# Kernel tuning notes

Hardware: AMD Instinct MI355X
Metric: run time of the kernel (lower is better)

## Reference

```python
import jax, jax.numpy as jnp
import numpy as np


def setup_inputs() -> dict:
    key = jax.random.key(0)
    kq, kk, kv = jax.random.split(key, 3)
    B, L, Q, H, E = 8, 128, 8, 8, 64
    S, P = 128, 8
    queries = jax.random.normal(kq, (B, L, Q, H, E), dtype=jnp.float32)
    keys = jax.random.normal(kk, (B, S, P, H, E), dtype=jnp.float32)
    values = jax.random.normal(kv, (B, S, P, H, E), dtype=jnp.float32)
    attn_mask = jnp.zeros((1,), dtype=bool)  # unused by the module
    return {"queries": queries, "keys": keys, "values": values, "attn_mask": attn_mask}


def reference(queries, keys, values, attn_mask):
    # queries: [B,L,Q,H,E]; keys/values: [B,S,P,H,E]
    B, L, Q, H, E = queries.shape
    S, P = values.shape[1], values.shape[2]
    scale = 1.0 / np.sqrt(E).astype(np.float32)
    # scores: [B,S,P,L,Q,H]
    scores = jnp.einsum('blqhe,bsphe->bsplqh', queries, keys)
    # softmax over joint (S,P) axis
    scaled = (scale * scores).reshape(B, S * P, L, Q, H)
    attn = jax.nn.softmax(scaled, axis=1).reshape(B, S, P, L, Q, H)
    # dropout is identity in eval / with p=0.0
    V = jnp.einsum('bsphe,bsplqh->blqhe', values, attn)
    return V
```

## Files before the change

kernel.cpp:

```cpp
#include <hip/hip_runtime.h>
#include <hip/hip_bf16.h>

typedef __attribute__((ext_vector_type(4))) float f32x4;
typedef __attribute__((ext_vector_type(16))) float f32x16;
typedef __attribute__((ext_vector_type(8))) short bf16x8;
typedef __attribute__((ext_vector_type(4))) unsigned u32x4;

#define MFMA32(a, b, c) __builtin_amdgcn_mfma_f32_32x32x16_bf16(a, b, c, 0, 0, 0)
#define EXP2(x) __builtin_amdgcn_exp2f(x)

constexpr int NQ = 1024;
constexpr int NK = 1024;
constexpr int RS = 512;
constexpr int Ec = 64;
constexpr int KT = 128;
constexpr int NT = NK / KT;
constexpr float QSCALE2 = 0.125f * 1.4426950408889634f;

__device__ __forceinline__ short f2bf(float x) {
    return (short)__builtin_bit_cast(unsigned short, __float2bfloat16(x));
}

__device__ __forceinline__ bf16x8 pack2(float4 a, float4 b) {
    bf16x8 r;
    r[0] = f2bf(a.x); r[1] = f2bf(a.y); r[2] = f2bf(a.z); r[3] = f2bf(a.w);
    r[4] = f2bf(b.x); r[5] = f2bf(b.y); r[6] = f2bf(b.z); r[7] = f2bf(b.w);
    return r;
}

__device__ __forceinline__ bf16x8 pack2s(float4 a, float4 b, float s) {
    bf16x8 r;
    r[0] = f2bf(a.x * s); r[1] = f2bf(a.y * s); r[2] = f2bf(a.z * s); r[3] = f2bf(a.w * s);
    r[4] = f2bf(b.x * s); r[5] = f2bf(b.y * s); r[6] = f2bf(b.z * s); r[7] = f2bf(b.w * s);
    return r;
}

__device__ __forceinline__ unsigned cvtpk(float a, float b) {
    unsigned lo = (unsigned short)__builtin_bit_cast(unsigned short, __float2bfloat16(a));
    unsigned hi = (unsigned short)__builtin_bit_cast(unsigned short, __float2bfloat16(b));
    return lo | (hi << 16);
}

__device__ __forceinline__ void gload16(const short* src, short* dst) {
    __builtin_amdgcn_global_load_lds((const __attribute__((address_space(1))) void*)src,
                                     (__attribute__((address_space(3))) void*)dst, 16, 0, 0);
}

__global__ __launch_bounds__(256, 4)
void cvt_kv(const float* __restrict__ Kg, const float* __restrict__ Vg,
            short* __restrict__ Kbf, short* __restrict__ Vt) {
    __shared__ __attribute__((aligned(16))) short Vl[64][72];
    const int tid  = threadIdx.x;
    const int head = blockIdx.x >> 4;
    const int kb   = blockIdx.x & 15;
    const int b    = head >> 3, h = head & 7;
    const int row  = tid >> 2, q = tid & 3;

    const size_t gin = (((size_t)(b * NK + kb * 64 + row)) * 8 + h) * 64 + q * 16;
    const float4* kp = (const float4*)(Kg + gin);
    float4 k0 = kp[0], k1 = kp[1], k2 = kp[2], k3 = kp[3];
    short* kout = Kbf + ((size_t)head * NK + kb * 64 + row) * 64 + q * 16;
    ((bf16x8*)kout)[0] = pack2(k0, k1);
    ((bf16x8*)kout)[1] = pack2(k2, k3);

    const float4* vp = (const float4*)(Vg + gin);
    float4 v0 = vp[0], v1 = vp[1], v2 = vp[2], v3 = vp[3];
    const float vv[16] = {v0.x, v0.y, v0.z, v0.w, v1.x, v1.y, v1.z, v1.w,
                          v2.x, v2.y, v2.z, v2.w, v3.x, v3.y, v3.z, v3.w};
#pragma unroll
    for (int j = 0; j < 16; ++j) Vl[q * 16 + j][row] = f2bf(vv[j]);
    __syncthreads();
    short* vout = Vt + ((size_t)head * Ec + row) * NK + kb * 64 + q * 16;
    ((bf16x8*)vout)[0] = *(const bf16x8*)&Vl[row][q * 16];
    ((bf16x8*)vout)[1] = *(const bf16x8*)&Vl[row][q * 16 + 8];
}

__global__ __launch_bounds__(512, 4)
void fully_attn_kernel(const float* __restrict__ Qg, const short* __restrict__ Kbf,
                       const short* __restrict__ Vt, float* __restrict__ Og) {
    __shared__ __attribute__((aligned(16))) short Kl[2][KT][64];
    __shared__ __attribute__((aligned(16))) short Vl[2][64][KT];

    const int tid  = threadIdx.x;
    const int lane = tid & 63;
    const int wv   = tid >> 6;
    const int grp  = wv & 3;
    const int par  = wv >> 2;
    const int ql   = lane & 31;
    const int hi   = lane >> 5;
    const int swz  = (lane & 7) << 4;

    const int bid  = blockIdx.x;
    const int head = (bid & 7) * 8 + (bid >> 6);
    const int qb   = (bid >> 3) & 7;
    const int b    = head >> 3, h = head & 7;

    const size_t headQ = (size_t)b * NQ * RS + (size_t)h * Ec;
    const short* Kh = Kbf + (size_t)head * NK * Ec;
    const short* Vh = Vt + (size_t)head * Ec * NK;

    const int qrow = qb * 128 + grp * 32 + ql;
    const float* qp = Qg + headQ + (size_t)qrow * RS;
    bf16x8 qf[4];
#pragma unroll
    for (int j = 0; j < 4; ++j) {
        const float4* q4 = (const float4*)(qp + j * 16 + hi * 8);
        qf[j] = pack2s(q4[0], q4[1], QSCALE2);
    }

    const int krow8 = lane >> 3;
    const int kj    = (lane & 7) ^ krow8;
    const int vrow4 = lane >> 4;

#define STAGE_K(buf, tt)                                                          \
    {                                                                             \
        _Pragma("unroll")                                                         \
        for (int s = 0; s < 2; ++s)                                               \
            gload16(Kh + (size_t)((tt) * KT + wv * 16 + s * 8 + krow8) * 64 +     \
                        kj * 8,                                                   \
                    &Kl[buf][wv * 16 + s * 8][0]);                                \
    }

#define STAGE_V(buf, tt)                                                          \
    {                                                                             \
        _Pragma("unroll")                                                         \
        for (int s = 0; s < 2; ++s)                                               \
            gload16(Vh + (size_t)(wv * 8 + s * 4 + vrow4) * NK + (tt) * KT +      \
                        (((lane & 15) ^ ((s * 4 + vrow4) & 7)) * 8),              \
                    &Vl[buf][wv * 8 + s * 4][0]);                                 \
    }

    STAGE_K(0, 0);
    STAGE_V(0, 0);
    __syncthreads();

    float l_r = 0.0f;
    f32x16 o0 = (f32x16)(0.0f), o1 = (f32x16)(0.0f);

    int cur = 0;
    for (int t = 0; t < NT; ++t) {
        if (t + 1 < NT) { STAGE_K(cur ^ 1, t + 1); STAGE_V(cur ^ 1, t + 1); }

        f32x16 p[2];
#pragma unroll
        for (int kt = 0; kt < 2; ++kt) {
            const char* kr = (const char*)&Kl[cur][par * 64 + kt * 32 + ql][0];
            bf16x8 kf0 = *(const bf16x8*)(kr + ((0 * 32 + hi * 16) ^ swz));
            bf16x8 kf1 = *(const bf16x8*)(kr + ((1 * 32 + hi * 16) ^ swz));
            bf16x8 kf2 = *(const bf16x8*)(kr + ((2 * 32 + hi * 16) ^ swz));
            bf16x8 kf3 = *(const bf16x8*)(kr + ((3 * 32 + hi * 16) ^ swz));
            __builtin_amdgcn_s_setprio(1);
            f32x16 acc = MFMA32(kf0, qf[0], (f32x16)(0.0f));
            acc = MFMA32(kf1, qf[1], acc);
            acc = MFMA32(kf2, qf[2], acc);
            acc = MFMA32(kf3, qf[3], acc);
            __builtin_amdgcn_s_setprio(0);
            p[kt] = acc;
        }

        float rs0 = 0.f, rs1 = 0.f, rs2 = 0.f, rs3 = 0.f;
#pragma unroll
        for (int kt = 0; kt < 2; ++kt)
#pragma unroll
            for (int i = 0; i < 16; i += 4) {
                float e0 = EXP2(p[kt][i + 0]);
                float e1 = EXP2(p[kt][i + 1]);
                float e2 = EXP2(p[kt][i + 2]);
                float e3 = EXP2(p[kt][i + 3]);
                p[kt][i + 0] = e0; p[kt][i + 1] = e1;
                p[kt][i + 2] = e2; p[kt][i + 3] = e3;
                rs0 += e0; rs1 += e1; rs2 += e2; rs3 += e3;
            }
        l_r += (rs0 + rs1) + (rs2 + rs3);

        const char* vr0 = (const char*)&Vl[cur][ql][0];
        const char* vr1 = (const char*)&Vl[cur][32 + ql][0];
        __builtin_amdgcn_s_setprio(1);
#pragma unroll
        for (int m = 0; m < 4; ++m) {
            const int kt = m >> 1, r0 = (m & 1) * 8;
            unsigned a0 = cvtpk(p[kt][r0 + 0], p[kt][r0 + 1]);
            unsigned a1 = cvtpk(p[kt][r0 + 2], p[kt][r0 + 3]);
            unsigned b0 = cvtpk(p[kt][r0 + 4], p[kt][r0 + 5]);
            unsigned b1 = cvtpk(p[kt][r0 + 6], p[kt][r0 + 7]);
            asm("v_permlane32_swap_b32 %0, %1" : "+v"(a0), "+v"(b0));
            asm("v_permlane32_swap_b32 %0, %1" : "+v"(a1), "+v"(b1));
            u32x4 w = {a0, a1, b0, b1};
            bf16x8 pf = __builtin_bit_cast(bf16x8, w);
            const int cb = (par * 128 + m * 32 + hi * 16) ^ swz;
            bf16x8 v0 = *(const bf16x8*)(vr0 + cb);
            bf16x8 v1 = *(const bf16x8*)(vr1 + cb);
            o0 = MFMA32(v0, pf, o0);
            o1 = MFMA32(v1, pf, o1);
        }
        __builtin_amdgcn_s_setprio(0);

        __syncthreads();
        cur ^= 1;
    }

    l_r += __shfl_xor(l_r, 32);

    float* scrO = (float*)&Kl[0][0][0];
    float* scrL = (float*)&Vl[0][0][0];
    const int slot = grp * 64 + lane;
    if (par == 1) {
#pragma unroll
        for (int i = 0; i < 16; ++i) {
            scrO[i * 256 + slot]        = o0[i];
            scrO[(16 + i) * 256 + slot] = o1[i];
        }
        scrL[slot] = l_r;
    }
    __syncthreads();
    if (par == 0) {
        const float inv = 1.0f / (l_r + scrL[slot]);
        float* op = Og + headQ + (size_t)qrow * RS;
#pragma unroll
        for (int bnk = 0; bnk < 4; ++bnk) {
            float4 s0, s1;
#pragma unroll
            for (int j = 0; j < 4; ++j) {
                const int i = bnk * 4 + j;
                ((float*)&s0)[j] = (o0[i] + scrO[i * 256 + slot]) * inv;
                ((float*)&s1)[j] = (o1[i] + scrO[(16 + i) * 256 + slot]) * inv;
            }
            *(float4*)(op + bnk * 8 + hi * 4)      = s0;
            *(float4*)(op + 32 + bnk * 8 + hi * 4) = s1;
        }
    }
}

extern "C" void kernel_launch(void* const* d_in, const int* in_sizes, int n_in,
                              void* d_out, int out_size, void* d_ws, size_t ws_size,
                              hipStream_t stream) {
    const float* Qg = (const float*)d_in[0];
    const float* Kg = (const float*)d_in[1];
    const float* Vg = (const float*)d_in[2];
    float* Og = (float*)d_out;

    short* Kbf = (short*)d_ws;
    short* Vt  = (short*)d_ws + (size_t)64 * NK * Ec;

    hipLaunchKernelGGL(cvt_kv, dim3(64 * 16), dim3(256), 0, stream, Kg, Vg, Kbf, Vt);
    hipLaunchKernelGGL(fully_attn_kernel, dim3(512), dim3(512), 0, stream,
                       Qg, Kbf, Vt, Og);
}
```

Baseline: 43.71 us.

## Process two query tiles per wave to reuse K/V fragments

Each wave now computes scores and outputs for two 32-row query tiles, sharing loaded K and V LDS fragments across both, and the grid halves to 256 blocks of 256 query rows. This reduces K/V staging and LDS reads per query row. It doubles accumulator registers, lowers occupancy to one block per CU, and enlarges the epilogue scratch, which may extend past the K buffer into the V buffer.

```diff
diff --git a/kernel.cpp b/kernel.cpp
--- a/kernel.cpp
+++ b/kernel.cpp
@@ -75,11 +75,12 @@
     ((bf16x8*)vout)[1] = *(const bf16x8*)&Vl[row][q * 16 + 8];
 }
 
-__global__ __launch_bounds__(512, 4)
+__global__ __launch_bounds__(512, 2)
 void fully_attn_kernel(const float* __restrict__ Qg, const short* __restrict__ Kbf,
                        const short* __restrict__ Vt, float* __restrict__ Og) {
     __shared__ __attribute__((aligned(16))) short Kl[2][KT][64];
     __shared__ __attribute__((aligned(16))) short Vl[2][64][KT];
+    __shared__ float scrL[512];
 
     const int tid  = threadIdx.x;
     const int lane = tid & 63;
@@ -91,21 +92,27 @@
     const int swz  = (lane & 7) << 4;
 
     const int bid  = blockIdx.x;
-    const int head = (bid & 7) * 8 + (bid >> 6);
-    const int qb   = (bid >> 3) & 7;
+    const int head = (bid & 7) * 8 + (bid >> 5);
+    const int qb   = (bid >> 3) & 3;
     const int b    = head >> 3, h = head & 7;
 
     const size_t headQ = (size_t)b * NQ * RS + (size_t)h * Ec;
     const short* Kh = Kbf + (size_t)head * NK * Ec;
     const short* Vh = Vt + (size_t)head * Ec * NK;
 
-    const int qrow = qb * 128 + grp * 32 + ql;
-    const float* qp = Qg + headQ + (size_t)qrow * RS;
-    bf16x8 qf[4];
-#pragma unroll
-    for (int j = 0; j < 4; ++j) {
-        const float4* q4 = (const float4*)(qp + j * 16 + hi * 8);
-        qf[j] = pack2s(q4[0], q4[1], QSCALE2);
+    const int qrowA = qb * 256 + grp * 64 + ql;
+    const int qrowB = qrowA + 32;
+    bf16x8 qfA[4], qfB[4];
+    {
+        const float* qpA = Qg + headQ + (size_t)qrowA * RS;
+        const float* qpB = Qg + headQ + (size_t)qrowB * RS;
+#pragma unroll
+        for (int j = 0; j < 4; ++j) {
+            const float4* a4 = (const float4*)(qpA + j * 16 + hi * 8);
+            const float4* b4 = (const float4*)(qpB + j * 16 + hi * 8);
+            qfA[j] = pack2s(a4[0], a4[1], QSCALE2);
+            qfB[j] = pack2s(b4[0], b4[1], QSCALE2);
+        }
     }
 
     const int krow8 = lane >> 3;
@@ -134,99 +141,152 @@
     STAGE_V(0, 0);
     __syncthreads();
 
-    float l_r = 0.0f;
-    f32x16 o0 = (f32x16)(0.0f), o1 = (f32x16)(0.0f);
+    float lA = 0.0f, lB = 0.0f;
+    f32x16 oA0 = (f32x16)(0.0f), oA1 = (f32x16)(0.0f);
+    f32x16 oB0 = (f32x16)(0.0f), oB1 = (f32x16)(0.0f);
 
     int cur = 0;
     for (int t = 0; t < NT; ++t) {
         if (t + 1 < NT) { STAGE_K(cur ^ 1, t + 1); STAGE_V(cur ^ 1, t + 1); }
 
-        f32x16 p[2];
+        bf16x8 kf[2][4];
 #pragma unroll
         for (int kt = 0; kt < 2; ++kt) {
             const char* kr = (const char*)&Kl[cur][par * 64 + kt * 32 + ql][0];
-            bf16x8 kf0 = *(const bf16x8*)(kr + ((0 * 32 + hi * 16) ^ swz));
-            bf16x8 kf1 = *(const bf16x8*)(kr + ((1 * 32 + hi * 16) ^ swz));
-            bf16x8 kf2 = *(const bf16x8*)(kr + ((2 * 32 + hi * 16) ^ swz));
-            bf16x8 kf3 = *(const bf16x8*)(kr + ((3 * 32 + hi * 16) ^ swz));
+#pragma unroll
+            for (int j = 0; j < 4; ++j)
+                kf[kt][j] = *(const bf16x8*)(kr + ((j * 32 + hi * 16) ^ swz));
+        }
+        f32x16 pA[2], pB[2];
+        __builtin_amdgcn_s_setprio(1);
+#pragma unroll
+        for (int kt = 0; kt < 2; ++kt) {
+            f32x16 a = (f32x16)(0.0f), bq = (f32x16)(0.0f);
+#pragma unroll
+            for (int j = 0; j < 4; ++j) {
+                a  = MFMA32(kf[kt][j], qfA[j], a);
+                bq = MFMA32(kf[kt][j], qfB[j], bq);
+            }
+            pA[kt] = a;
+            pB[kt] = bq;
+        }
+        __builtin_amdgcn_s_setprio(0);
+
+        bf16x8 vf0[4], vf1[4];
+#pragma unroll
+        for (int m = 0; m < 4; ++m) {
+            const int cb = (par * 128 + m * 32 + hi * 16) ^ swz;
+            vf0[m] = *(const bf16x8*)((const char*)&Vl[cur][ql][0] + cb);
+            vf1[m] = *(const bf16x8*)((const char*)&Vl[cur][32 + ql][0] + cb);
+        }
+
+        {
+            float rs0 = 0.f, rs1 = 0.f, rs2 = 0.f, rs3 = 0.f;
+#pragma unroll
+            for (int kt = 0; kt < 2; ++kt)
+#pragma unroll
+                for (int i = 0; i < 16; i += 4) {
+                    float e0 = EXP2(pA[kt][i + 0]);
+                    float e1 = EXP2(pA[kt][i + 1]);
+                    float e2 = EXP2(pA[kt][i + 2]);
+                    float e3 = EXP2(pA[kt][i + 3]);
+                    pA[kt][i + 0] = e0; pA[kt][i + 1] = e1;
+                    pA[kt][i + 2] = e2; pA[kt][i + 3] = e3;
+                    rs0 += e0; rs1 += e1; rs2 += e2; rs3 += e3;
+                }
+            lA += (rs0 + rs1) + (rs2 + rs3);
             __builtin_amdgcn_s_setprio(1);
-            f32x16 acc = MFMA32(kf0, qf[0], (f32x16)(0.0f));
-            acc = MFMA32(kf1, qf[1], acc);
-            acc = MFMA32(kf2, qf[2], acc);
-            acc = MFMA32(kf3, qf[3], acc);
+#pragma unroll
+            for (int m = 0; m < 4; ++m) {
+                const int kt = m >> 1, r0 = (m & 1) * 8;
+                unsigned a0 = cvtpk(pA[kt][r0 + 0], pA[kt][r0 + 1]);
+                unsigned a1 = cvtpk(pA[kt][r0 + 2], pA[kt][r0 + 3]);
+                unsigned b0 = cvtpk(pA[kt][r0 + 4], pA[kt][r0 + 5]);
+                unsigned b1 = cvtpk(pA[kt][r0 + 6], pA[kt][r0 + 7]);
+                asm("v_permlane32_swap_b32 %0, %1" : "+v"(a0), "+v"(b0));
+                asm("v_permlane32_swap_b32 %0, %1" : "+v"(a1), "+v"(b1));
+                u32x4 w = {a0, a1, b0, b1};
+                bf16x8 pf = __builtin_bit_cast(bf16x8, w);
+                oA0 = MFMA32(vf0[m], pf, oA0);
+                oA1 = MFMA32(vf1[m], pf, oA1);
+            }
             __builtin_amdgcn_s_setprio(0);
-            p[kt] = acc;
-        }
-
-        float rs0 = 0.f, rs1 = 0.f, rs2 = 0.f, rs3 = 0.f;
-#pragma unroll
-        for (int kt = 0; kt < 2; ++kt)
-#pragma unroll
-            for (int i = 0; i < 16; i += 4) {
-                float e0 = EXP2(p[kt][i + 0]);
-                float e1 = EXP2(p[kt][i + 1]);
-                float e2 = EXP2(p[kt][i + 2]);
-                float e3 = EXP2(p[kt][i + 3]);
-                p[kt][i + 0] = e0; p[kt][i + 1] = e1;
-                p[kt][i + 2] = e2; p[kt][i + 3] = e3;
-                rs0 += e0; rs1 += e1; rs2 += e2; rs3 += e3;
+        }
+
+        {
+            float rs0 = 0.f, rs1 = 0.f, rs2 = 0.f, rs3 = 0.f;
+#pragma unroll
+            for (int kt = 0; kt < 2; ++kt)
+#pragma unroll
+                for (int i = 0; i < 16; i += 4) {
+                    float e0 = EXP2(pB[kt][i + 0]);
+                    float e1 = EXP2(pB[kt][i + 1]);
+                    float e2 = EXP2(pB[kt][i + 2]);
+                    float e3 = EXP2(pB[kt][i + 3]);
+                    pB[kt][i + 0] = e0; pB[kt][i + 1] = e1;
+                    pB[kt][i + 2] = e2; pB[kt][i + 3] = e3;
+                    rs0 += e0; rs1 += e1; rs2 += e2; rs3 += e3;
+                }
+            lB += (rs0 + rs1) + (rs2 + rs3);
+            __builtin_amdgcn_s_setprio(1);
+#pragma unroll
+            for (int m = 0; m < 4; ++m) {
+                const int kt = m >> 1, r0 = (m & 1) * 8;
+                unsigned a0 = cvtpk(pB[kt][r0 + 0], pB[kt][r0 + 1]);
+                unsigned a1 = cvtpk(pB[kt][r0 + 2], pB[kt][r0 + 3]);
+                unsigned b0 = cvtpk(pB[kt][r0 + 4], pB[kt][r0 + 5]);
+                unsigned b1 = cvtpk(pB[kt][r0 + 6], pB[kt][r0 + 7]);
+                asm("v_permlane32_swap_b32 %0, %1" : "+v"(a0), "+v"(b0));
+                asm("v_permlane32_swap_b32 %0, %1" : "+v"(a1), "+v"(b1));
+                u32x4 w = {a0, a1, b0, b1};
+                bf16x8 pf = __builtin_bit_cast(bf16x8, w);
+                oB0 = MFMA32(vf0[m], pf, oB0);
+                oB1 = MFMA32(vf1[m], pf, oB1);
             }
-        l_r += (rs0 + rs1) + (rs2 + rs3);
-
-        const char* vr0 = (const char*)&Vl[cur][ql][0];
-        const char* vr1 = (const char*)&Vl[cur][32 + ql][0];
-        __builtin_amdgcn_s_setprio(1);
-#pragma unroll
-        for (int m = 0; m < 4; ++m) {
-            const int kt = m >> 1, r0 = (m & 1) * 8;
-            unsigned a0 = cvtpk(p[kt][r0 + 0], p[kt][r0 + 1]);
-            unsigned a1 = cvtpk(p[kt][r0 + 2], p[kt][r0 + 3]);
-            unsigned b0 = cvtpk(p[kt][r0 + 4], p[kt][r0 + 5]);
-            unsigned b1 = cvtpk(p[kt][r0 + 6], p[kt][r0 + 7]);
-            asm("v_permlane32_swap_b32 %0, %1" : "+v"(a0), "+v"(b0));
-            asm("v_permlane32_swap_b32 %0, %1" : "+v"(a1), "+v"(b1));
-            u32x4 w = {a0, a1, b0, b1};
-            bf16x8 pf = __builtin_bit_cast(bf16x8, w);
-            const int cb = (par * 128 + m * 32 + hi * 16) ^ swz;
-            bf16x8 v0 = *(const bf16x8*)(vr0 + cb);
-            bf16x8 v1 = *(const bf16x8*)(vr1 + cb);
-            o0 = MFMA32(v0, pf, o0);
-            o1 = MFMA32(v1, pf, o1);
-        }
-        __builtin_amdgcn_s_setprio(0);
+            __builtin_amdgcn_s_setprio(0);
+        }
 
         __syncthreads();
         cur ^= 1;
     }
 
-    l_r += __shfl_xor(l_r, 32);
-
-    float* scrO = (float*)&Kl[0][0][0];
-    float* scrL = (float*)&Vl[0][0][0];
-    const int slot = grp * 64 + lane;
+    lA += __shfl_xor(lA, 32);
+    lB += __shfl_xor(lB, 32);
+
+    float* scr = (float*)&Kl[0][0][0];
+    const int qslotA = grp * 64 + ql;
+    const int qslotB = qslotA + 32;
     if (par == 1) {
 #pragma unroll
         for (int i = 0; i < 16; ++i) {
-            scrO[i * 256 + slot]        = o0[i];
-            scrO[(16 + i) * 256 + slot] = o1[i];
-        }
-        scrL[slot] = l_r;
+            scr[(hi * 16 + i) * 256 + qslotA]      = oA0[i];
+            scr[(32 + hi * 16 + i) * 256 + qslotA] = oA1[i];
+            scr[(hi * 16 + i) * 256 + qslotB]      = oB0[i];
+            scr[(32 + hi * 16 + i) * 256 + qslotB] = oB1[i];
+        }
+        if (hi == 0) { scrL[qslotA] = lA; scrL[qslotB] = lB; }
     }
     __syncthreads();
     if (par == 0) {
-        const float inv = 1.0f / (l_r + scrL[slot]);
-        float* op = Og + headQ + (size_t)qrow * RS;
+        const float invA = 1.0f / (lA + scrL[qslotA]);
+        const float invB = 1.0f / (lB + scrL[qslotB]);
+        float* opA = Og + headQ + (size_t)qrowA * RS;
+        float* opB = Og + headQ + (size_t)qrowB * RS;
 #pragma unroll
         for (int bnk = 0; bnk < 4; ++bnk) {
-            float4 s0, s1;
+            float4 sA0, sA1, sB0, sB1;
 #pragma unroll
             for (int j = 0; j < 4; ++j) {
                 const int i = bnk * 4 + j;
-                ((float*)&s0)[j] = (o0[i] + scrO[i * 256 + slot]) * inv;
-                ((float*)&s1)[j] = (o1[i] + scrO[(16 + i) * 256 + slot]) * inv;
+                ((float*)&sA0)[j] = (oA0[i] + scr[(hi * 16 + i) * 256 + qslotA]) * invA;
+                ((float*)&sA1)[j] = (oA1[i] + scr[(32 + hi * 16 + i) * 256 + qslotA]) * invA;
+                ((float*)&sB0)[j] = (oB0[i] + scr[(hi * 16 + i) * 256 + qslotB]) * invB;
+                ((float*)&sB1)[j] = (oB1[i] + scr[(32 + hi * 16 + i) * 256 + qslotB]) * invB;
             }
-            *(float4*)(op + bnk * 8 + hi * 4)      = s0;
-            *(float4*)(op + 32 + bnk * 8 + hi * 4) = s1;
+            *(float4*)(opA + bnk * 8 + hi * 4)      = sA0;
+            *(float4*)(opA + 32 + bnk * 8 + hi * 4) = sA1;
+            *(float4*)(opB + bnk * 8 + hi * 4)      = sB0;
+            *(float4*)(opB + 32 + bnk * 8 + hi * 4) = sB1;
         }
     }
 }
@@ -243,6 +303,6 @@
     short* Vt  = (short*)d_ws + (size_t)64 * NK * Ec;
 
     hipLaunchKernelGGL(cvt_kv, dim3(64 * 16), dim3(256), 0, stream, Kg, Vg, Kbf, Vt);
-    hipLaunchKernelGGL(fully_attn_kernel, dim3(512), dim3(512), 0, stream,
+    hipLaunchKernelGGL(fully_attn_kernel, dim3(256), dim3(512), 0, stream,
                        Qg, Kbf, Vt, Og);
 }
```

New measurement: 45.31 us. +3.7%, slower.
